# Kernel optimization log

Measured on AMD Instinct MI355X. Metric: run time of the kernel, lower is better.

## Reference

```python
import jax, jax.numpy as jnp
import numpy as np

N_NODES = 10000

def _gcn_norm(edges, n_nodes):
    # PyG GCNConv default: add self-loops, symmetric normalization D^-1/2 A_hat D^-1/2
    src, dst = edges[0], edges[1]
    loop = jnp.arange(n_nodes, dtype=src.dtype)
    src = jnp.concatenate([src, loop])
    dst = jnp.concatenate([dst, loop])
    deg = jax.ops.segment_sum(jnp.ones_like(dst, dtype=jnp.float32), dst, num_segments=n_nodes)
    dinv = jnp.where(deg > 0, jax.lax.rsqrt(deg), 0.0)
    norm = dinv[src] * dinv[dst]  # [E + N]
    return src, dst, norm

def _gcn_layer(x, src, dst, norm, W, b):
    # linear transform, then gather -> weight -> scatter-add aggregation
    x = x @ W  # [N, F]
    msg = x[src] * norm[:, None]  # [E+N, F]
    out = jax.ops.segment_sum(msg, dst, num_segments=x.shape[0])
    return out + b

def setup_inputs() -> dict:
    key = jax.random.key(0)
    k1, k2, k3, k4 = jax.random.split(key, 4)
    d = 128
    E = 640000
    scale = 1.0 / np.sqrt(d)
    return {
        "nodes_embeddings": jax.random.normal(k1, (N_NODES, d), dtype=jnp.float32),
        "edges": jax.random.randint(k2, (2, E), 0, N_NODES, dtype=jnp.int64),
        "W1": jax.random.normal(k3, (d, d), dtype=jnp.float32) * scale,
        "b1": jnp.zeros((d,), dtype=jnp.float32),
        "W2": jax.random.normal(k4, (d, d), dtype=jnp.float32) * scale,
        "b2": jnp.zeros((d,), dtype=jnp.float32),
    }

def reference(nodes_embeddings, edges, W1, b1, W2, b2):
    src, dst, norm = _gcn_norm(edges, nodes_embeddings.shape[0])
    x = _gcn_layer(nodes_embeddings, src, dst, norm, W1, b1)
    x = _gcn_layer(x, src, dst, norm, W2, b2)
    return x
```

## Files before the change

kernel.cpp:

```cpp
#include <hip/hip_runtime.h>
#include <hip/hip_bf16.h>

#define D 128
#define NBINS 157
#define BIN_CAP 5120
#define EPB 4096

__device__ __forceinline__ unsigned rne_bf16(float f) {
    unsigned u = __float_as_uint(f);
    return (u + 0x7FFFu + ((u >> 16) & 1u)) >> 16;
}
__device__ __forceinline__ float bf16_lo(unsigned u) { return __uint_as_float(u << 16); }
__device__ __forceinline__ float bf16_hi(unsigned u) { return __uint_as_float(u & 0xFFFF0000u); }

__global__ __launch_bounds__(512) void fused_gemm_scatter(
        const float* __restrict__ X, const float* __restrict__ W,
        float* __restrict__ Y,
        const int* __restrict__ src, const int* __restrict__ dst,
        int* __restrict__ binTotal, int* __restrict__ binned,
        int E, int N, int gGemm) {
    __shared__ float smem[D * D];
    int tid = threadIdx.x;

    if ((int)blockIdx.x < gGemm) {
        {
            const float4* W4 = (const float4*)W;
            float4* Ws4 = (float4*)smem;
            #pragma unroll
            for (int i = 0; i < 8; ++i)
                Ws4[tid + 512 * i] = W4[tid + 512 * i];
        }
        __syncthreads();
        const float2* Ws2 = (const float2*)smem;
        int col2 = tid & 63;
        int wv   = __builtin_amdgcn_readfirstlane(tid >> 6);
        int row0 = blockIdx.x * 32 + wv * 4;
        if (row0 >= N) return;

        const float4* xr[4];
        #pragma unroll
        for (int r = 0; r < 4; ++r) {
            int rr = row0 + r; if (rr > N - 1) rr = N - 1;
            xr[r] = (const float4*)(X + (size_t)rr * D);
        }
        float accx[4] = {0.f, 0.f, 0.f, 0.f};
        float accy[4] = {0.f, 0.f, 0.f, 0.f};
        #pragma unroll 8
        for (int kb = 0; kb < 32; ++kb) {
            float4 xv[4];
            #pragma unroll
            for (int r = 0; r < 4; ++r) xv[r] = xr[r][kb];
            #pragma unroll
            for (int kk = 0; kk < 4; ++kk) {
                float2 w = Ws2[(4 * kb + kk) * 64 + col2];
                #pragma unroll
                for (int r = 0; r < 4; ++r) {
                    float xs = ((const float*)&xv[r])[kk];
                    accx[r] = fmaf(xs, w.x, accx[r]);
                    accy[r] = fmaf(xs, w.y, accy[r]);
                }
            }
        }
        #pragma unroll
        for (int r = 0; r < 4; ++r) {
            int rr = row0 + r;
            if (rr < N)
                ((float2*)Y)[(size_t)rr * 64 + col2] = make_float2(accx[r], accy[r]);
        }
    } else {
        int* cnt   = (int*)smem;
        int* loff  = cnt + 160;
        int* gbase = cnt + 320;
        int* scur  = cnt + 480;
        int* stage = cnt + 640;
        for (int b = tid; b < NBINS; b += 512) cnt[b] = 0;
        __syncthreads();

        int bid = blockIdx.x - gGemm;
        int base = bid * EPB + tid * 8;
        int s[8], dl[8], bn[8];
        int ne = 0;
        if (base + 8 <= E) {
            const int4* s4 = (const int4*)(src + base);
            const int4* d4 = (const int4*)(dst + base);
            int4 a0 = s4[0], a1 = s4[1], c0 = d4[0], c1 = d4[1];
            int ss[8] = {a0.x, a0.y, a0.z, a0.w, a1.x, a1.y, a1.z, a1.w};
            int dd[8] = {c0.x, c0.y, c0.z, c0.w, c1.x, c1.y, c1.z, c1.w};
            ne = 8;
            #pragma unroll
            for (int i = 0; i < 8; ++i) { s[i] = ss[i]; bn[i] = dd[i] >> 6; dl[i] = dd[i] & 63; }
        } else {
            for (int i = 0; i < 8; ++i) {
                int e = base + i;
                if (e < E) { s[ne] = src[e]; int d = dst[e]; bn[ne] = d >> 6; dl[ne] = d & 63; ++ne; }
            }
        }
        for (int i = 0; i < ne; ++i) atomicAdd(&cnt[bn[i]], 1);
        __syncthreads();

        if (tid < NBINS) gbase[tid] = atomicAdd(&binTotal[tid], cnt[tid]);
        if (tid < 64) {
            int c0 = (3 * tid     < NBINS) ? cnt[3 * tid    ] : 0;
            int c1 = (3 * tid + 1 < NBINS) ? cnt[3 * tid + 1] : 0;
            int c2 = (3 * tid + 2 < NBINS) ? cnt[3 * tid + 2] : 0;
            int tsum = c0 + c1 + c2;
            int incl = tsum;
            #pragma unroll
            for (int off = 1; off < 64; off <<= 1) {
                int t = __shfl_up(incl, off);
                if (tid >= off) incl += t;
            }
            int excl = incl - tsum;
            if (3 * tid     < NBINS) loff[3 * tid    ] = excl;
            if (3 * tid + 1 < NBINS) loff[3 * tid + 1] = excl + c0;
            if (3 * tid + 2 < NBINS) loff[3 * tid + 2] = excl + c0 + c1;
        }
        __syncthreads();
        if (tid < NBINS) scur[tid] = loff[tid];
        __syncthreads();

        for (int i = 0; i < ne; ++i) {
            int p = atomicAdd(&scur[bn[i]], 1);
            stage[p] = s[i] | (dl[i] << 14);
        }
        __syncthreads();

        int wv = tid >> 6, lane = tid & 63;
        for (int b = wv; b < NBINS; b += 8) {
            int n = cnt[b], so = loff[b], go = b * BIN_CAP + gbase[b];
            for (int i = lane; i < n; i += 64) binned[go + i] = stage[so + i];
        }
    }
}

__global__ __launch_bounds__(256) void sort_bins(const int* __restrict__ binTotal,
                                                 const int* __restrict__ binned,
                                                 unsigned short* __restrict__ csr16,
                                                 float* __restrict__ dinv,
                                                 int* __restrict__ nodeStart,
                                                 int* __restrict__ nodeEnd,
                                                 const float* __restrict__ Y,
                                                 unsigned* __restrict__ Zb, int N) {
    __shared__ int h[4][64];
    __shared__ int cur[4][64];
    __shared__ float sdinv[64];
    __shared__ int padTot;
    __shared__ int stage[BIN_CAP];
    int b = blockIdx.x, tid = threadIdx.x;
    int wv = tid >> 6, lane = tid & 63;
    int cntb = binTotal[b];
    h[wv][lane] = 0;
    __syncthreads();
    const int* bp = binned + b * BIN_CAP;
    for (int i = tid; i < cntb; i += 256) atomicAdd(&h[wv][bp[i] >> 14], 1);
    __syncthreads();
    if (tid < 64) {
        int d0 = h[0][tid], d1 = h[1][tid], d2 = h[2][tid], d3 = h[3][tid];
        int deg = d0 + d1 + d2 + d3;
        int pdeg = (deg + 7) & ~7;
        int incl = pdeg;
        #pragma unroll
        for (int off = 1; off < 64; off <<= 1) {
            int t = __shfl_up(incl, off);
            if (tid >= off) incl += t;
        }
        int excl = incl - pdeg;
        cur[0][tid] = excl;
        cur[1][tid] = excl + d0;
        cur[2][tid] = excl + d0 + d1;
        cur[3][tid] = excl + d0 + d1 + d2;
        float dv = rsqrtf((float)(deg + 1));
        sdinv[tid] = dv;
        if (tid == 63) padTot = incl;
        int node = b * 64 + tid;
        if (node < N) {
            dinv[node]      = dv;
            nodeStart[node] = b * BIN_CAP + excl;
            nodeEnd[node]   = b * BIN_CAP + excl + pdeg;
        }
    }
    __syncthreads();
    int cntPad = padTot;
    for (int i = tid; i < cntPad; i += 256) stage[i] = N;
    __syncthreads();
    for (int i = tid; i < cntb; i += 256) {
        int p = bp[i];
        int pos = atomicAdd(&cur[wv][p >> 14], 1);
        stage[pos] = p & 0x3FFF;
    }
    {
        const float4* Y4 = (const float4*)Y;
        uint2* Zb2 = (uint2*)Zb;
        #pragma unroll
        for (int i = 0; i < 8; ++i) {
            int idx = tid + 256 * i;
            int row = idx >> 5, c = idx & 31;
            int node = b * 64 + row;
            if (node < N) {
                float4 v = Y4[(size_t)node * 32 + c];
                float dv = sdinv[row];
                uint2 o;
                o.x = (rne_bf16(v.y * dv) << 16) | rne_bf16(v.x * dv);
                o.y = (rne_bf16(v.w * dv) << 16) | rne_bf16(v.z * dv);
                Zb2[(size_t)node * 32 + c] = o;
            }
        }
    }
    if (b == 0 && tid < 64) Zb[(size_t)N * 64 + tid] = 0u;
    __syncthreads();
    unsigned short* bw = csr16 + b * BIN_CAP;
    for (int i = tid; i < cntPad; i += 256) bw[i] = (unsigned short)stage[i];
}

__global__ __launch_bounds__(256) void gemm_scale(const float* __restrict__ X,
                                                  const float* __restrict__ W,
                                                  const float* __restrict__ dinv,
                                                  unsigned* __restrict__ Zb, int N) {
    __shared__ float Ws[D * D];
    {
        const float4* W4 = (const float4*)W;
        float4* Ws4 = (float4*)Ws;
        #pragma unroll
        for (int i = 0; i < 16; ++i)
            Ws4[threadIdx.x + 256 * i] = W4[threadIdx.x + 256 * i];
    }
    __syncthreads();
    const float2* Ws2 = (const float2*)Ws;
    int col2 = threadIdx.x & 63;
    int wv   = __builtin_amdgcn_readfirstlane(threadIdx.x >> 6);
    int row0 = blockIdx.x * 16 + wv * 4;
    if (row0 >= N) return;

    const float4* xr[4];
    #pragma unroll
    for (int r = 0; r < 4; ++r) {
        int rr = row0 + r; if (rr > N - 1) rr = N - 1;
        xr[r] = (const float4*)(X + (size_t)rr * D);
    }
    float accx[4] = {0.f, 0.f, 0.f, 0.f};
    float accy[4] = {0.f, 0.f, 0.f, 0.f};
    #pragma unroll 8
    for (int kb = 0; kb < 32; ++kb) {
        float4 xv[4];
        #pragma unroll
        for (int r = 0; r < 4; ++r) xv[r] = xr[r][kb];
        #pragma unroll
        for (int kk = 0; kk < 4; ++kk) {
            float2 w = Ws2[(4 * kb + kk) * 64 + col2];
            #pragma unroll
            for (int r = 0; r < 4; ++r) {
                float xs = ((const float*)&xv[r])[kk];
                accx[r] = fmaf(xs, w.x, accx[r]);
                accy[r] = fmaf(xs, w.y, accy[r]);
            }
        }
    }
    #pragma unroll
    for (int r = 0; r < 4; ++r) {
        int rr = row0 + r;
        if (rr < N) {
            float dv = dinv[rr];
            Zb[(size_t)rr * 64 + col2] =
                (rne_bf16(accy[r] * dv) << 16) | rne_bf16(accx[r] * dv);
        }
    }
}

__global__ __launch_bounds__(256) void aggregate(const unsigned* __restrict__ Zb,
                                                 const int* __restrict__ nodeStart,
                                                 const int* __restrict__ nodeEnd,
                                                 const unsigned short* __restrict__ csr16,
                                                 const float* __restrict__ dinv,
                                                 const float* __restrict__ bias,
                                                 float* __restrict__ Out, int N) {
    int wv    = __builtin_amdgcn_readfirstlane(threadIdx.x >> 6);
    int nodeA = blockIdx.x * 8 + wv * 2;
    if (nodeA >= N) return;
    int nodeB = nodeA + 1;
    bool hasB = (nodeB < N);
    int lane = threadIdx.x & 63;
    int g    = lane >> 4;
    int l16  = lane & 15;

    const uint4* Z4 = (const uint4*)Zb;
    float a0=0.f,a1=0.f,a2=0.f,a3=0.f,a4=0.f,a5=0.f,a6=0.f,a7=0.f;
    float b0=0.f,b1v=0.f,b2v=0.f,b3=0.f,b4v=0.f,b5=0.f,b6=0.f,b7=0.f;

    int eA = nodeStart[nodeA], endA = nodeEnd[nodeA];
    int eB = 0, endB = 0;
    if (hasB) { eB = nodeStart[nodeB]; endB = nodeEnd[nodeB]; }

    while (eA < endA || eB < endB) {
        int remA = endA - eA; int cntA = remA > 64 ? 64 : (remA > 0 ? remA : 0);
        int remB = endB - eB; int cntB = remB > 64 ? 64 : (remB > 0 ? remB : 0);
        int myA = (lane < cntA) ? (int)csr16[eA + lane] : N;
        int myB = (lane < cntB) ? (int)csr16[eB + lane] : N;
        int cmax = cntA > cntB ? cntA : cntB;
        int rounds = cmax >> 2;
        #pragma unroll 16
        for (int j = 0; j < rounds; ++j) {
            int idxA = __shfl(myA, j * 4 + g);
            int idxB = __shfl(myB, j * 4 + g);
            uint4 ua = Z4[idxA * 16 + l16];
            uint4 ub = Z4[idxB * 16 + l16];
            a0 += bf16_lo(ua.x); a1 += bf16_hi(ua.x);
            a2 += bf16_lo(ua.y); a3 += bf16_hi(ua.y);
            a4 += bf16_lo(ua.z); a5 += bf16_hi(ua.z);
            a6 += bf16_lo(ua.w); a7 += bf16_hi(ua.w);
            b0  += bf16_lo(ub.x); b1v += bf16_hi(ub.x);
            b2v += bf16_lo(ub.y); b3  += bf16_hi(ub.y);
            b4v += bf16_lo(ub.z); b5  += bf16_hi(ub.z);
            b6  += bf16_lo(ub.w); b7  += bf16_hi(ub.w);
        }
        eA += cntA; eB += cntB;
    }
    #pragma unroll
    for (int m = 16; m <= 32; m <<= 1) {
        a0 += __shfl_xor(a0, m); a1 += __shfl_xor(a1, m);
        a2 += __shfl_xor(a2, m); a3 += __shfl_xor(a3, m);
        a4 += __shfl_xor(a4, m); a5 += __shfl_xor(a5, m);
        a6 += __shfl_xor(a6, m); a7 += __shfl_xor(a7, m);
        b0  += __shfl_xor(b0, m);  b1v += __shfl_xor(b1v, m);
        b2v += __shfl_xor(b2v, m); b3  += __shfl_xor(b3, m);
        b4v += __shfl_xor(b4v, m); b5  += __shfl_xor(b5, m);
        b6  += __shfl_xor(b6, m);  b7  += __shfl_xor(b7, m);
    }
    int half = lane >> 4;
    if (half == 0 || (half == 1 && hasB)) {
        int node = half ? nodeB : nodeA;
        float r0 = half ? b0  : a0, r1 = half ? b1v : a1;
        float r2 = half ? b2v : a2, r3 = half ? b3  : a3;
        float r4 = half ? b4v : a4, r5 = half ? b5  : a5;
        float r6 = half ? b6  : a6, r7 = half ? b7  : a7;
        uint4 su = Z4[node * 16 + l16];
        float dv = dinv[node];
        const float4* bp4 = (const float4*)bias;
        float4 ba = bp4[l16 * 2], bb = bp4[l16 * 2 + 1];
        float4 o0, o1;
        o0.x = (r0 + bf16_lo(su.x)) * dv + ba.x;
        o0.y = (r1 + bf16_hi(su.x)) * dv + ba.y;
        o0.z = (r2 + bf16_lo(su.y)) * dv + ba.z;
        o0.w = (r3 + bf16_hi(su.y)) * dv + ba.w;
        o1.x = (r4 + bf16_lo(su.z)) * dv + bb.x;
        o1.y = (r5 + bf16_hi(su.z)) * dv + bb.y;
        o1.z = (r6 + bf16_lo(su.w)) * dv + bb.z;
        o1.w = (r7 + bf16_hi(su.w)) * dv + bb.w;
        float4* op = (float4*)Out + (size_t)node * 32 + l16 * 2;
        op[0] = o0;
        op[1] = o1;
    }
}

extern "C" void kernel_launch(void* const* d_in, const int* in_sizes, int n_in,
                              void* d_out, int out_size, void* d_ws, size_t ws_size,
                              hipStream_t stream) {
    const float* X  = (const float*)d_in[0];
    const int*   ed = (const int*)d_in[1];
    const float* W1 = (const float*)d_in[2];
    const float* b1 = (const float*)d_in[3];
    const float* W2 = (const float*)d_in[4];
    const float* b2 = (const float*)d_in[5];
    float* out = (float*)d_out;

    const int N = in_sizes[0] / D;
    const int E = in_sizes[1] / 2;
    const int* src = ed;
    const int* dst = ed + E;

    char* w = (char*)d_ws;
    float*    Y        = (float*)w;            w += (size_t)N * D * sizeof(float);
    unsigned* Zb       = (unsigned*)w;         w += (size_t)(N + 1) * 64 * sizeof(unsigned);
    int*      binned   = (int*)w;              w += (size_t)NBINS * BIN_CAP * sizeof(int);
    unsigned short* csr16 = (unsigned short*)w; w += (size_t)NBINS * BIN_CAP * sizeof(unsigned short);
    float*    dinv     = (float*)w;            w += (size_t)N * sizeof(float);
    int*      nodeStart= (int*)w;              w += (size_t)N * sizeof(int);
    int*      nodeEnd  = (int*)w;              w += (size_t)N * sizeof(int);
    int*      binTotal = (int*)w;              w += (size_t)NBINS * sizeof(int);

    hipMemsetAsync(binTotal, 0, NBINS * sizeof(int), stream);

    int gGemm1 = (N + 31) / 32;
    int gScat  = (E + EPB - 1) / EPB;
    fused_gemm_scatter<<<gGemm1 + gScat, 512, 0, stream>>>(
        X, W1, Y, src, dst, binTotal, binned, E, N, gGemm1);
    sort_bins<<<NBINS, 256, 0, stream>>>(binTotal, binned, csr16, dinv,
                                         nodeStart, nodeEnd, Y, Zb, N);

    int gAgg = (N + 7) / 8;
    aggregate<<<gAgg, 256, 0, stream>>>(Zb, nodeStart, nodeEnd, csr16, dinv, b1, out, N);

    int gGemm2 = (N + 15) / 16;
    gemm_scale<<<gGemm2, 256, 0, stream>>>(out, W2, dinv, Zb, N);
    aggregate<<<gAgg, 256, 0, stream>>>(Zb, nodeStart, nodeEnd, csr16, dinv, b2, out, N);
}
```

Before: 140.4 us.

## Pipeline aggregate gathers through LDS ring with async global_load_lds

Rewrites the aggregate kernel so each wave stages its two nodes' edge lists into LDS, then streams neighbor feature rows into an 8-slot LDS ring buffer using direct global-to-LDS loads, keeping 7 loads in flight. Each half-wave now handles one node, with two edges per round, so accumulator registers are halved and the cross-lane reduction shrinks to one shuffle step. The goal is more memory-level parallelism on the irregular gathers. It adds LDS use and manual vmcnt waits, and nodes with more than 128 edges fall back to a plain global-load loop.

Result: slower. 160.6 us (+14.3%).

```diff
diff --git a/kernel.cpp b/kernel.cpp
--- a/kernel.cpp
+++ b/kernel.cpp
@@ -12,6 +12,15 @@
 }
 __device__ __forceinline__ float bf16_lo(unsigned u) { return __uint_as_float(u << 16); }
 __device__ __forceinline__ float bf16_hi(unsigned u) { return __uint_as_float(u & 0xFFFF0000u); }
+
+__device__ __forceinline__ void gload_lds16(const void* g, void* l) {
+    __builtin_amdgcn_global_load_lds((const __attribute__((address_space(1))) void*)g,
+                                     (__attribute__((address_space(3))) void*)l, 16, 0, 0);
+}
+__device__ __forceinline__ void gload_lds4(const void* g, void* l) {
+    __builtin_amdgcn_global_load_lds((const __attribute__((address_space(1))) void*)g,
+                                     (__attribute__((address_space(3))) void*)l, 4, 0, 0);
+}
 
 __global__ __launch_bounds__(512) void fused_gemm_scatter(
         const float* __restrict__ X, const float* __restrict__ W,
@@ -266,6 +275,9 @@
     }
 }
 
+#define AGG_D 7
+#define ECAP 128
+
 __global__ __launch_bounds__(256) void aggregate(const unsigned* __restrict__ Zb,
                                                  const int* __restrict__ nodeStart,
                                                  const int* __restrict__ nodeEnd,
@@ -273,78 +285,102 @@
                                                  const float* __restrict__ dinv,
                                                  const float* __restrict__ bias,
                                                  float* __restrict__ Out, int N) {
-    int wv    = __builtin_amdgcn_readfirstlane(threadIdx.x >> 6);
+    __shared__ unsigned ring[4][8][256];
+    __shared__ unsigned short eL[4][2][ECAP];
+    int tid  = threadIdx.x;
+    int wv   = __builtin_amdgcn_readfirstlane(tid >> 6);
+    int lane = tid & 63;
     int nodeA = blockIdx.x * 8 + wv * 2;
     if (nodeA >= N) return;
     int nodeB = nodeA + 1;
     bool hasB = (nodeB < N);
-    int lane = threadIdx.x & 63;
-    int g    = lane >> 4;
-    int l16  = lane & 15;
+
+    int eA = nodeStart[nodeA], cA = nodeEnd[nodeA] - eA;
+    int eB = eA, cB = 0;
+    if (hasB) { eB = nodeStart[nodeB]; cB = nodeEnd[nodeB] - eB; }
+
+    gload_lds4(csr16 + eA + 2 * lane, &eL[wv][0][0]);
+    gload_lds4(csr16 + eB + 2 * lane, &eL[wv][1][0]);
+    asm volatile("s_waitcnt vmcnt(0)" ::: "memory");
+
+    int cAc = cA > ECAP ? ECAP : cA;
+    int cBc = cB > ECAP ? ECAP : cB;
+    int cmax = cAc > cBc ? cAc : cBc;
+    for (int k = cAc + lane; k < cmax; k += 64) eL[wv][0][k] = (unsigned short)N;
+    for (int k = cBc + lane; k < cmax; k += 64) eL[wv][1][k] = (unsigned short)N;
+    int R = cmax >> 1;
+
+    int l16   = lane & 15;
+    int phalf = (lane >> 4) & 1;
+    int nhalf = lane >> 5;
+    const unsigned short* myList = &eL[wv][nhalf][0];
+    const char* zbase = (const char*)Zb + (l16 << 4);
+
+    float f0=0.f,f1=0.f,f2=0.f,f3=0.f,f4=0.f,f5=0.f,f6=0.f,f7=0.f;
+
+    int P = R < AGG_D ? R : AGG_D;
+    for (int j = 0; j < P; ++j) {
+        int row = myList[2 * j + phalf];
+        gload_lds16(zbase + ((size_t)row << 8), &ring[wv][j & 7][0]);
+    }
+    int RD = R - AGG_D; if (RD < 0) RD = 0;
+    for (int i = 0; i < RD; ++i) {
+        int j = i + AGG_D;
+        int row = myList[2 * j + phalf];
+        gload_lds16(zbase + ((size_t)row << 8), &ring[wv][j & 7][0]);
+        asm volatile("s_waitcnt vmcnt(7)" ::: "memory");
+        uint4 v = *(const uint4*)&ring[wv][i & 7][lane * 4];
+        f0 += bf16_lo(v.x); f1 += bf16_hi(v.x);
+        f2 += bf16_lo(v.y); f3 += bf16_hi(v.y);
+        f4 += bf16_lo(v.z); f5 += bf16_hi(v.z);
+        f6 += bf16_lo(v.w); f7 += bf16_hi(v.w);
+    }
+    asm volatile("s_waitcnt vmcnt(0)" ::: "memory");
+    for (int i = RD; i < R; ++i) {
+        uint4 v = *(const uint4*)&ring[wv][i & 7][lane * 4];
+        f0 += bf16_lo(v.x); f1 += bf16_hi(v.x);
+        f2 += bf16_lo(v.y); f3 += bf16_hi(v.y);
+        f4 += bf16_lo(v.z); f5 += bf16_hi(v.z);
+        f6 += bf16_lo(v.w); f7 += bf16_hi(v.w);
+    }
 
     const uint4* Z4 = (const uint4*)Zb;
-    float a0=0.f,a1=0.f,a2=0.f,a3=0.f,a4=0.f,a5=0.f,a6=0.f,a7=0.f;
-    float b0=0.f,b1v=0.f,b2v=0.f,b3=0.f,b4v=0.f,b5=0.f,b6=0.f,b7=0.f;
-
-    int eA = nodeStart[nodeA], endA = nodeEnd[nodeA];
-    int eB = 0, endB = 0;
-    if (hasB) { eB = nodeStart[nodeB]; endB = nodeEnd[nodeB]; }
-
-    while (eA < endA || eB < endB) {
-        int remA = endA - eA; int cntA = remA > 64 ? 64 : (remA > 0 ? remA : 0);
-        int remB = endB - eB; int cntB = remB > 64 ? 64 : (remB > 0 ? remB : 0);
-        int myA = (lane < cntA) ? (int)csr16[eA + lane] : N;
-        int myB = (lane < cntB) ? (int)csr16[eB + lane] : N;
-        int cmax = cntA > cntB ? cntA : cntB;
-        int rounds = cmax >> 2;
-        #pragma unroll 16
-        for (int j = 0; j < rounds; ++j) {
-            int idxA = __shfl(myA, j * 4 + g);
-            int idxB = __shfl(myB, j * 4 + g);
-            uint4 ua = Z4[idxA * 16 + l16];
-            uint4 ub = Z4[idxB * 16 + l16];
-            a0 += bf16_lo(ua.x); a1 += bf16_hi(ua.x);
-            a2 += bf16_lo(ua.y); a3 += bf16_hi(ua.y);
-            a4 += bf16_lo(ua.z); a5 += bf16_hi(ua.z);
-            a6 += bf16_lo(ua.w); a7 += bf16_hi(ua.w);
-            b0  += bf16_lo(ub.x); b1v += bf16_hi(ub.x);
-            b2v += bf16_lo(ub.y); b3  += bf16_hi(ub.y);
-            b4v += bf16_lo(ub.z); b5  += bf16_hi(ub.z);
-            b6  += bf16_lo(ub.w); b7  += bf16_hi(ub.w);
-        }
-        eA += cntA; eB += cntB;
-    }
-    #pragma unroll
-    for (int m = 16; m <= 32; m <<= 1) {
-        a0 += __shfl_xor(a0, m); a1 += __shfl_xor(a1, m);
-        a2 += __shfl_xor(a2, m); a3 += __shfl_xor(a3, m);
-        a4 += __shfl_xor(a4, m); a5 += __shfl_xor(a5, m);
-        a6 += __shfl_xor(a6, m); a7 += __shfl_xor(a7, m);
-        b0  += __shfl_xor(b0, m);  b1v += __shfl_xor(b1v, m);
-        b2v += __shfl_xor(b2v, m); b3  += __shfl_xor(b3, m);
-        b4v += __shfl_xor(b4v, m); b5  += __shfl_xor(b5, m);
-        b6  += __shfl_xor(b6, m);  b7  += __shfl_xor(b7, m);
-    }
+    int cmaxF = cA > cB ? cA : cB;
+    if (cmaxF > ECAP) {
+        int eX = nhalf ? eB : eA;
+        int cX = nhalf ? cB : cA;
+        for (int j = ECAP >> 1; j < (cmaxF >> 1); ++j) {
+            int q = 2 * j + phalf;
+            int row = (q < cX) ? (int)csr16[eX + q] : N;
+            uint4 v = Z4[(size_t)row * 16 + l16];
+            f0 += bf16_lo(v.x); f1 += bf16_hi(v.x);
+            f2 += bf16_lo(v.y); f3 += bf16_hi(v.y);
+            f4 += bf16_lo(v.z); f5 += bf16_hi(v.z);
+            f6 += bf16_lo(v.w); f7 += bf16_hi(v.w);
+        }
+    }
+
+    f0 += __shfl_xor(f0, 16); f1 += __shfl_xor(f1, 16);
+    f2 += __shfl_xor(f2, 16); f3 += __shfl_xor(f3, 16);
+    f4 += __shfl_xor(f4, 16); f5 += __shfl_xor(f5, 16);
+    f6 += __shfl_xor(f6, 16); f7 += __shfl_xor(f7, 16);
+
     int half = lane >> 4;
-    if (half == 0 || (half == 1 && hasB)) {
-        int node = half ? nodeB : nodeA;
-        float r0 = half ? b0  : a0, r1 = half ? b1v : a1;
-        float r2 = half ? b2v : a2, r3 = half ? b3  : a3;
-        float r4 = half ? b4v : a4, r5 = half ? b5  : a5;
-        float r6 = half ? b6  : a6, r7 = half ? b7  : a7;
-        uint4 su = Z4[node * 16 + l16];
+    if (half == 0 || (half == 2 && hasB)) {
+        int node = (half == 2) ? nodeB : nodeA;
+        uint4 su = Z4[(size_t)node * 16 + l16];
         float dv = dinv[node];
         const float4* bp4 = (const float4*)bias;
         float4 ba = bp4[l16 * 2], bb = bp4[l16 * 2 + 1];
         float4 o0, o1;
-        o0.x = (r0 + bf16_lo(su.x)) * dv + ba.x;
-        o0.y = (r1 + bf16_hi(su.x)) * dv + ba.y;
-        o0.z = (r2 + bf16_lo(su.y)) * dv + ba.z;
-        o0.w = (r3 + bf16_hi(su.y)) * dv + ba.w;
-        o1.x = (r4 + bf16_lo(su.z)) * dv + bb.x;
-        o1.y = (r5 + bf16_hi(su.z)) * dv + bb.y;
-        o1.z = (r6 + bf16_lo(su.w)) * dv + bb.z;
-        o1.w = (r7 + bf16_hi(su.w)) * dv + bb.w;
+        o0.x = (f0 + bf16_lo(su.x)) * dv + ba.x;
+        o0.y = (f1 + bf16_hi(su.x)) * dv + ba.y;
+        o0.z = (f2 + bf16_lo(su.y)) * dv + ba.z;
+        o0.w = (f3 + bf16_hi(su.y)) * dv + ba.w;
+        o1.x = (f4 + bf16_lo(su.z)) * dv + bb.x;
+        o1.y = (f5 + bf16_hi(su.z)) * dv + bb.y;
+        o1.z = (f6 + bf16_lo(su.w)) * dv + bb.z;
+        o1.w = (f7 + bf16_hi(su.w)) * dv + bb.w;
         float4* op = (float4*)Out + (size_t)node * 32 + l16 * 2;
         op[0] = o0;
         op[1] = o1;
```

## Fuse layer-2 GEMM into the first aggregate kernel epilogue

Applied to the files above, without the earlier changes.

The first aggregation kernel now stages its 8 output rows in LDS and multiplies them by W2 directly, writing dinv-scaled bf16 features into a second Z buffer. This removes the separate gemm_scale launch and the fp32 round trip of the intermediate layer output through global memory. In exchange each aggregate block reads all of W2 from global or L2 (uncached in LDS) for its 8 rows, adds a block-wide sync, and a second Z buffer is needed so layer 1's gather input is not overwritten while the same launch still reads it.

After: 140.8 us. No clear change (+0.3%).

```diff
diff --git a/kernel.cpp b/kernel.cpp
--- a/kernel.cpp
+++ b/kernel.cpp
@@ -140,7 +140,8 @@
                                                  int* __restrict__ nodeStart,
                                                  int* __restrict__ nodeEnd,
                                                  const float* __restrict__ Y,
-                                                 unsigned* __restrict__ Zb, int N) {
+                                                 unsigned* __restrict__ Zb,
+                                                 unsigned* __restrict__ Zb2, int N) {
     __shared__ int h[4][64];
     __shared__ int cur[4][64];
     __shared__ float sdinv[64];
@@ -190,7 +191,7 @@
     }
     {
         const float4* Y4 = (const float4*)Y;
-        uint2* Zb2 = (uint2*)Zb;
+        uint2* Zb2v = (uint2*)Zb;
         #pragma unroll
         for (int i = 0; i < 8; ++i) {
             int idx = tid + 256 * i;
@@ -202,68 +203,17 @@
                 uint2 o;
                 o.x = (rne_bf16(v.y * dv) << 16) | rne_bf16(v.x * dv);
                 o.y = (rne_bf16(v.w * dv) << 16) | rne_bf16(v.z * dv);
-                Zb2[(size_t)node * 32 + c] = o;
-            }
-        }
-    }
-    if (b == 0 && tid < 64) Zb[(size_t)N * 64 + tid] = 0u;
+                Zb2v[(size_t)node * 32 + c] = o;
+            }
+        }
+    }
+    if (b == 0 && tid < 64) {
+        Zb [(size_t)N * 64 + tid] = 0u;
+        Zb2[(size_t)N * 64 + tid] = 0u;
+    }
     __syncthreads();
     unsigned short* bw = csr16 + b * BIN_CAP;
     for (int i = tid; i < cntPad; i += 256) bw[i] = (unsigned short)stage[i];
-}
-
-__global__ __launch_bounds__(256) void gemm_scale(const float* __restrict__ X,
-                                                  const float* __restrict__ W,
-                                                  const float* __restrict__ dinv,
-                                                  unsigned* __restrict__ Zb, int N) {
-    __shared__ float Ws[D * D];
-    {
-        const float4* W4 = (const float4*)W;
-        float4* Ws4 = (float4*)Ws;
-        #pragma unroll
-        for (int i = 0; i < 16; ++i)
-            Ws4[threadIdx.x + 256 * i] = W4[threadIdx.x + 256 * i];
-    }
-    __syncthreads();
-    const float2* Ws2 = (const float2*)Ws;
-    int col2 = threadIdx.x & 63;
-    int wv   = __builtin_amdgcn_readfirstlane(threadIdx.x >> 6);
-    int row0 = blockIdx.x * 16 + wv * 4;
-    if (row0 >= N) return;
-
-    const float4* xr[4];
-    #pragma unroll
-    for (int r = 0; r < 4; ++r) {
-        int rr = row0 + r; if (rr > N - 1) rr = N - 1;
-        xr[r] = (const float4*)(X + (size_t)rr * D);
-    }
-    float accx[4] = {0.f, 0.f, 0.f, 0.f};
-    float accy[4] = {0.f, 0.f, 0.f, 0.f};
-    #pragma unroll 8
-    for (int kb = 0; kb < 32; ++kb) {
-        float4 xv[4];
-        #pragma unroll
-        for (int r = 0; r < 4; ++r) xv[r] = xr[r][kb];
-        #pragma unroll
-        for (int kk = 0; kk < 4; ++kk) {
-            float2 w = Ws2[(4 * kb + kk) * 64 + col2];
-            #pragma unroll
-            for (int r = 0; r < 4; ++r) {
-                float xs = ((const float*)&xv[r])[kk];
-                accx[r] = fmaf(xs, w.x, accx[r]);
-                accy[r] = fmaf(xs, w.y, accy[r]);
-            }
-        }
-    }
-    #pragma unroll
-    for (int r = 0; r < 4; ++r) {
-        int rr = row0 + r;
-        if (rr < N) {
-            float dv = dinv[rr];
-            Zb[(size_t)rr * 64 + col2] =
-                (rne_bf16(accy[r] * dv) << 16) | rne_bf16(accx[r] * dv);
-        }
-    }
 }
 
 __global__ __launch_bounds__(256) void aggregate(const unsigned* __restrict__ Zb,
@@ -272,82 +222,122 @@
                                                  const unsigned short* __restrict__ csr16,
                                                  const float* __restrict__ dinv,
                                                  const float* __restrict__ bias,
-                                                 float* __restrict__ Out, int N) {
+                                                 float* __restrict__ Out, int N,
+                                                 const float* __restrict__ W2,
+                                                 unsigned* __restrict__ Zout) {
+    __shared__ float rowsLds[8][128];
+    const bool fused = (W2 != nullptr);
     int wv    = __builtin_amdgcn_readfirstlane(threadIdx.x >> 6);
     int nodeA = blockIdx.x * 8 + wv * 2;
-    if (nodeA >= N) return;
-    int nodeB = nodeA + 1;
-    bool hasB = (nodeB < N);
+    bool active = (nodeA < N);
+    if (!fused && !active) return;
     int lane = threadIdx.x & 63;
-    int g    = lane >> 4;
     int l16  = lane & 15;
 
-    const uint4* Z4 = (const uint4*)Zb;
-    float a0=0.f,a1=0.f,a2=0.f,a3=0.f,a4=0.f,a5=0.f,a6=0.f,a7=0.f;
-    float b0=0.f,b1v=0.f,b2v=0.f,b3=0.f,b4v=0.f,b5=0.f,b6=0.f,b7=0.f;
-
-    int eA = nodeStart[nodeA], endA = nodeEnd[nodeA];
-    int eB = 0, endB = 0;
-    if (hasB) { eB = nodeStart[nodeB]; endB = nodeEnd[nodeB]; }
-
-    while (eA < endA || eB < endB) {
-        int remA = endA - eA; int cntA = remA > 64 ? 64 : (remA > 0 ? remA : 0);
-        int remB = endB - eB; int cntB = remB > 64 ? 64 : (remB > 0 ? remB : 0);
-        int myA = (lane < cntA) ? (int)csr16[eA + lane] : N;
-        int myB = (lane < cntB) ? (int)csr16[eB + lane] : N;
-        int cmax = cntA > cntB ? cntA : cntB;
-        int rounds = cmax >> 2;
-        #pragma unroll 16
-        for (int j = 0; j < rounds; ++j) {
-            int idxA = __shfl(myA, j * 4 + g);
-            int idxB = __shfl(myB, j * 4 + g);
-            uint4 ua = Z4[idxA * 16 + l16];
-            uint4 ub = Z4[idxB * 16 + l16];
-            a0 += bf16_lo(ua.x); a1 += bf16_hi(ua.x);
-            a2 += bf16_lo(ua.y); a3 += bf16_hi(ua.y);
-            a4 += bf16_lo(ua.z); a5 += bf16_hi(ua.z);
-            a6 += bf16_lo(ua.w); a7 += bf16_hi(ua.w);
-            b0  += bf16_lo(ub.x); b1v += bf16_hi(ub.x);
-            b2v += bf16_lo(ub.y); b3  += bf16_hi(ub.y);
-            b4v += bf16_lo(ub.z); b5  += bf16_hi(ub.z);
-            b6  += bf16_lo(ub.w); b7  += bf16_hi(ub.w);
-        }
-        eA += cntA; eB += cntB;
-    }
-    #pragma unroll
-    for (int m = 16; m <= 32; m <<= 1) {
-        a0 += __shfl_xor(a0, m); a1 += __shfl_xor(a1, m);
-        a2 += __shfl_xor(a2, m); a3 += __shfl_xor(a3, m);
-        a4 += __shfl_xor(a4, m); a5 += __shfl_xor(a5, m);
-        a6 += __shfl_xor(a6, m); a7 += __shfl_xor(a7, m);
-        b0  += __shfl_xor(b0, m);  b1v += __shfl_xor(b1v, m);
-        b2v += __shfl_xor(b2v, m); b3  += __shfl_xor(b3, m);
-        b4v += __shfl_xor(b4v, m); b5  += __shfl_xor(b5, m);
-        b6  += __shfl_xor(b6, m);  b7  += __shfl_xor(b7, m);
-    }
-    int half = lane >> 4;
-    if (half == 0 || (half == 1 && hasB)) {
-        int node = half ? nodeB : nodeA;
-        float r0 = half ? b0  : a0, r1 = half ? b1v : a1;
-        float r2 = half ? b2v : a2, r3 = half ? b3  : a3;
-        float r4 = half ? b4v : a4, r5 = half ? b5  : a5;
-        float r6 = half ? b6  : a6, r7 = half ? b7  : a7;
-        uint4 su = Z4[node * 16 + l16];
-        float dv = dinv[node];
-        const float4* bp4 = (const float4*)bias;
-        float4 ba = bp4[l16 * 2], bb = bp4[l16 * 2 + 1];
-        float4 o0, o1;
-        o0.x = (r0 + bf16_lo(su.x)) * dv + ba.x;
-        o0.y = (r1 + bf16_hi(su.x)) * dv + ba.y;
-        o0.z = (r2 + bf16_lo(su.y)) * dv + ba.z;
-        o0.w = (r3 + bf16_hi(su.y)) * dv + ba.w;
-        o1.x = (r4 + bf16_lo(su.z)) * dv + bb.x;
-        o1.y = (r5 + bf16_hi(su.z)) * dv + bb.y;
-        o1.z = (r6 + bf16_lo(su.w)) * dv + bb.z;
-        o1.w = (r7 + bf16_hi(su.w)) * dv + bb.w;
-        float4* op = (float4*)Out + (size_t)node * 32 + l16 * 2;
-        op[0] = o0;
-        op[1] = o1;
+    if (active) {
+        int nodeB = nodeA + 1;
+        bool hasB = (nodeB < N);
+        int g = lane >> 4;
+
+        const uint4* Z4 = (const uint4*)Zb;
+        float a0=0.f,a1=0.f,a2=0.f,a3=0.f,a4=0.f,a5=0.f,a6=0.f,a7=0.f;
+        float b0=0.f,b1v=0.f,b2v=0.f,b3=0.f,b4v=0.f,b5=0.f,b6=0.f,b7=0.f;
+
+        int eA = nodeStart[nodeA], endA = nodeEnd[nodeA];
+        int eB = 0, endB = 0;
+        if (hasB) { eB = nodeStart[nodeB]; endB = nodeEnd[nodeB]; }
+
+        while (eA < endA || eB < endB) {
+            int remA = endA - eA; int cntA = remA > 64 ? 64 : (remA > 0 ? remA : 0);
+            int remB = endB - eB; int cntB = remB > 64 ? 64 : (remB > 0 ? remB : 0);
+            int myA = (lane < cntA) ? (int)csr16[eA + lane] : N;
+            int myB = (lane < cntB) ? (int)csr16[eB + lane] : N;
+            int cmax = cntA > cntB ? cntA : cntB;
+            int rounds = cmax >> 2;
+            #pragma unroll 16
+            for (int j = 0; j < rounds; ++j) {
+                int idxA = __shfl(myA, j * 4 + g);
+                int idxB = __shfl(myB, j * 4 + g);
+                uint4 ua = Z4[idxA * 16 + l16];
+                uint4 ub = Z4[idxB * 16 + l16];
+                a0 += bf16_lo(ua.x); a1 += bf16_hi(ua.x);
+                a2 += bf16_lo(ua.y); a3 += bf16_hi(ua.y);
+                a4 += bf16_lo(ua.z); a5 += bf16_hi(ua.z);
+                a6 += bf16_lo(ua.w); a7 += bf16_hi(ua.w);
+                b0  += bf16_lo(ub.x); b1v += bf16_hi(ub.x);
+                b2v += bf16_lo(ub.y); b3  += bf16_hi(ub.y);
+                b4v += bf16_lo(ub.z); b5  += bf16_hi(ub.z);
+                b6  += bf16_lo(ub.w); b7  += bf16_hi(ub.w);
+            }
+            eA += cntA; eB += cntB;
+        }
+        #pragma unroll
+        for (int m = 16; m <= 32; m <<= 1) {
+            a0 += __shfl_xor(a0, m); a1 += __shfl_xor(a1, m);
+            a2 += __shfl_xor(a2, m); a3 += __shfl_xor(a3, m);
+            a4 += __shfl_xor(a4, m); a5 += __shfl_xor(a5, m);
+            a6 += __shfl_xor(a6, m); a7 += __shfl_xor(a7, m);
+            b0  += __shfl_xor(b0, m);  b1v += __shfl_xor(b1v, m);
+            b2v += __shfl_xor(b2v, m); b3  += __shfl_xor(b3, m);
+            b4v += __shfl_xor(b4v, m); b5  += __shfl_xor(b5, m);
+            b6  += __shfl_xor(b6, m);  b7  += __shfl_xor(b7, m);
+        }
+        int half = lane >> 4;
+        if (half == 0 || (half == 1 && hasB)) {
+            int node = half ? nodeB : nodeA;
+            float r0 = half ? b0  : a0, r1 = half ? b1v : a1;
+            float r2 = half ? b2v : a2, r3 = half ? b3  : a3;
+            float r4 = half ? b4v : a4, r5 = half ? b5  : a5;
+            float r6 = half ? b6  : a6, r7 = half ? b7  : a7;
+            uint4 su = Z4[node * 16 + l16];
+            float dv = dinv[node];
+            const float4* bp4 = (const float4*)bias;
+            float4 ba = bp4[l16 * 2], bb = bp4[l16 * 2 + 1];
+            float4 o0, o1;
+            o0.x = (r0 + bf16_lo(su.x)) * dv + ba.x;
+            o0.y = (r1 + bf16_hi(su.x)) * dv + ba.y;
+            o0.z = (r2 + bf16_lo(su.y)) * dv + ba.z;
+            o0.w = (r3 + bf16_hi(su.y)) * dv + ba.w;
+            o1.x = (r4 + bf16_lo(su.z)) * dv + bb.x;
+            o1.y = (r5 + bf16_hi(su.z)) * dv + bb.y;
+            o1.z = (r6 + bf16_lo(su.w)) * dv + bb.z;
+            o1.w = (r7 + bf16_hi(su.w)) * dv + bb.w;
+            if (fused) {
+                float4* rp = (float4*)&rowsLds[wv * 2 + half][0];
+                rp[l16 * 2]     = o0;
+                rp[l16 * 2 + 1] = o1;
+            } else {
+                float4* op = (float4*)Out + (size_t)node * 32 + l16 * 2;
+                op[0] = o0;
+                op[1] = o1;
+            }
+        }
+    }
+
+    if (fused) {
+        __syncthreads();
+        int tid  = threadIdx.x;
+        int colg = (tid & 31) << 2;
+        int r    = tid >> 5;
+        int node = blockIdx.x * 8 + r;
+        const float* xrow = &rowsLds[r][0];
+        float ac0 = 0.f, ac1 = 0.f, ac2 = 0.f, ac3 = 0.f;
+        #pragma unroll 8
+        for (int k = 0; k < 128; ++k) {
+            float xs = xrow[k];
+            float4 w4 = *(const float4*)(W2 + (size_t)k * D + colg);
+            ac0 = fmaf(xs, w4.x, ac0);
+            ac1 = fmaf(xs, w4.y, ac1);
+            ac2 = fmaf(xs, w4.z, ac2);
+            ac3 = fmaf(xs, w4.w, ac3);
+        }
+        if (node < N) {
+            float dv = dinv[node];
+            uint2 o;
+            o.x = (rne_bf16(ac1 * dv) << 16) | rne_bf16(ac0 * dv);
+            o.y = (rne_bf16(ac3 * dv) << 16) | rne_bf16(ac2 * dv);
+            ((uint2*)Zout)[(size_t)node * 32 + (colg >> 2)] = o;
+        }
     }
 }
 
@@ -370,6 +360,7 @@
     char* w = (char*)d_ws;
     float*    Y        = (float*)w;            w += (size_t)N * D * sizeof(float);
     unsigned* Zb       = (unsigned*)w;         w += (size_t)(N + 1) * 64 * sizeof(unsigned);
+    unsigned* Zb2      = (unsigned*)w;         w += (size_t)(N + 1) * 64 * sizeof(unsigned);
     int*      binned   = (int*)w;              w += (size_t)NBINS * BIN_CAP * sizeof(int);
     unsigned short* csr16 = (unsigned short*)w; w += (size_t)NBINS * BIN_CAP * sizeof(unsigned short);
     float*    dinv     = (float*)w;            w += (size_t)N * sizeof(float);
@@ -384,12 +375,11 @@
     fused_gemm_scatter<<<gGemm1 + gScat, 512, 0, stream>>>(
         X, W1, Y, src, dst, binTotal, binned, E, N, gGemm1);
     sort_bins<<<NBINS, 256, 0, stream>>>(binTotal, binned, csr16, dinv,
-                                         nodeStart, nodeEnd, Y, Zb, N);
+                                         nodeStart, nodeEnd, Y, Zb, Zb2, N);
 
     int gAgg = (N + 7) / 8;
-    aggregate<<<gAgg, 256, 0, stream>>>(Zb, nodeStart, nodeEnd, csr16, dinv, b1, out, N);
-
-    int gGemm2 = (N + 15) / 16;
-    gemm_scale<<<gGemm2, 256, 0, stream>>>(out, W2, dinv, Zb, N);
-    aggregate<<<gAgg, 256, 0, stream>>>(Zb, nodeStart, nodeEnd, csr16, dinv, b2, out, N);
-}
+    aggregate<<<gAgg, 256, 0, stream>>>(Zb, nodeStart, nodeEnd, csr16, dinv,
+                                        b1, out, N, W2, Zb2);
+    aggregate<<<gAgg, 256, 0, stream>>>(Zb2, nodeStart, nodeEnd, csr16, dinv,
+                                        b2, out, N, nullptr, nullptr);
+}
```
